# Performance work log

Measured on AMD Instinct MI355X. Metric: run time of the kernel, lower is better.

The kernel has to match this reference:

```python
import jax, jax.numpy as jnp
import numpy as np

N, CH = 65536, 256
B, K, CTX = 8, 256, 768
H, D = 8, 64
NPB = N // B  # points per batch (scene)


def setup_inputs() -> dict:
    key = jax.random.key(0)
    ks = jax.random.split(key, 8)
    xF = jax.random.normal(ks[0], (N, CH), dtype=jnp.float32)
    context = jax.random.normal(ks[1], (B, K, CTX), dtype=jnp.float32)
    # decomposition_permutations: a random partition of the N sparse points into B groups
    perm = jax.random.permutation(ks[2], N).reshape(B, NPB).astype(jnp.int32)
    Wq = jax.random.normal(ks[3], (CH, H * D), dtype=jnp.float32) * 0.02
    Wk = jax.random.normal(ks[4], (CTX, H * D), dtype=jnp.float32) * 0.02
    Wv = jax.random.normal(ks[5], (CTX, H * D), dtype=jnp.float32) * 0.02
    Wout = jax.random.normal(ks[6], (H * D, CH), dtype=jnp.float32) * 0.02
    b_out = jnp.zeros((CH,), dtype=jnp.float32)
    return {"xF": xF, "context": context, "perm": perm,
            "Wq": Wq, "Wk": Wk, "Wv": Wv, "Wout": Wout, "b_out": b_out}


def reference(xF, context, perm, Wq, Wk, Wv, Wout, b_out):
    scale = D ** -0.5
    q = (xF @ Wq).reshape(N, H, D)                     # to_q (1x1 conv == linear)
    k = (context @ Wk).reshape(B, K, H, D)             # to_k
    v = (context @ Wv).reshape(B, K, H, D)             # to_v
    qg = q[perm]                                        # gather: [B, NPB, H, D]
    attn = jax.nn.softmax(scale * jnp.einsum('bqhd,bkhd->bhqk', qg, k), axis=-1)
    o = jnp.einsum('bhqk,bkhd->bqhd', attn, v).reshape(B * NPB, H * D)
    # inverse-permutation scatter back to sparse-tensor order: ft[inv_perm]
    ft = jnp.zeros((N, H * D), o.dtype).at[perm.reshape(-1)].set(o)
    out = ft @ Wout + b_out                             # to_out
    return out + xF                                     # residual
```

## Files before the change

### kernel.cpp

```cpp
#include <hip/hip_runtime.h>

typedef unsigned short u16;
typedef __attribute__((ext_vector_type(8))) short bf16x8;
typedef __attribute__((ext_vector_type(4))) float f32x4;
typedef __attribute__((ext_vector_type(4))) int i32x4;
typedef __attribute__((ext_vector_type(2))) int i32x2;

#define N_PTS   65536
#define CH_DIM  256
#define BATCH   8
#define KTOK    256
#define CTX_DIM 768
#define NHEAD   8
#define HD      64
#define HDIM    512
#define NPB     8192

__device__ __forceinline__ u16 f2bf(float f) {
    union { float f; unsigned u; } v; v.f = f;
    unsigned r = v.u + 0x7fffu + ((v.u >> 16) & 1u);
    return (u16)(r >> 16);
}
__device__ __forceinline__ unsigned cvtpk(float lo, float hi) {
    unsigned r;
    asm("v_cvt_pk_bf16_f32 %0, %1, %2" : "=v"(r) : "v"(lo), "v"(hi));
    return r;
}
__device__ __forceinline__ float exp2_hw(float x) {
    float r;
    asm("v_exp_f32 %0, %1" : "=v"(r) : "v"(x));
    return r;
}

__device__ __forceinline__ void gll16(const void* g, void* l) {
    __builtin_amdgcn_global_load_lds(
        (const __attribute__((address_space(1))) void*)g,
        (__attribute__((address_space(3))) void*)l, 16, 0, 0);
}

__global__ void convk(const float* __restrict__ src, u16* __restrict__ dst, int n8) {
    int i = blockIdx.x * blockDim.x + threadIdx.x;
    int st = gridDim.x * blockDim.x;
    for (; i < n8; i += st) {
        const float* p = src + (size_t)i * 8;
        f32x4 a = *(const f32x4*)p;
        f32x4 b = *(const f32x4*)(p + 4);
        i32x4 o;
        o[0] = (int)cvtpk(a[0], a[1]);
        o[1] = (int)cvtpk(a[2], a[3]);
        o[2] = (int)cvtpk(b[0], b[1]);
        o[3] = (int)cvtpk(b[2], b[3]);
        *(i32x4*)&dst[(size_t)i * 8] = o;
    }
}

__global__ void tconvk(const float* __restrict__ W, u16* __restrict__ WT, int R, int C) {
    int i = blockIdx.x * blockDim.x + threadIdx.x;
    if (i >= R * C) return;
    int c = i / R, r = i - c * R;
    WT[(size_t)c * R + r] = f2bf(W[(size_t)r * C + c]);
}

template <bool OUT_F32, bool VT_OUT>
__global__ __launch_bounds__(256, 3) void gemm_bt(
    const u16* __restrict__ A, const u16* __restrict__ BT, void* __restrict__ Cv,
    int M, int N, int K,
    const float* __restrict__ bias, const float* __restrict__ resid, float oscale)
{
    __shared__ __align__(16) u16 As[128 * 32];
    __shared__ __align__(16) u16 Bs[128 * 32];

    const int tid  = threadIdx.x;
    const int lane = tid & 63;
    const int w    = tid >> 6;
    const int wm   = w & 1;
    const int wn   = w >> 1;

    const int nwg = gridDim.x * gridDim.y;
    const int wg  = blockIdx.y * gridDim.x + blockIdx.x;
    const int swz = (wg & 7) * (nwg >> 3) + (wg >> 3);
    const int n0  = (swz % gridDim.x) * 128;
    const int m0  = (swz / gridDim.x) * 128;

    const int l15  = lane & 15;
    const int quad = lane >> 4;

    f32x4 acc[4][4];
#pragma unroll
    for (int i = 0; i < 4; i++)
#pragma unroll
        for (int j = 0; j < 4; j++) { acc[i][j][0]=0.f; acc[i][j][1]=0.f; acc[i][j][2]=0.f; acc[i][j][3]=0.f; }

    const int sr = tid >> 2;
    const int sc = (tid & 3) * 8;
    const u16* Abase = A  + (size_t)(m0 + sr) * K + sc;
    const u16* Bbase = BT + (size_t)(n0 + sr) * K + sc;
    u16* AsD = &As[tid * 8];
    u16* BsD = &Bs[tid * 8];
    const size_t rowStep = (size_t)64 * K;

    for (int k0 = 0; k0 < K; k0 += 32) {
        gll16(Abase + k0,           AsD);
        gll16(Abase + k0 + rowStep, AsD + 2048);
        gll16(Bbase + k0,           BsD);
        gll16(Bbase + k0 + rowStep, BsD + 2048);
        __syncthreads();

        bf16x8 af[4], bfr[4];
#pragma unroll
        for (int rt = 0; rt < 4; rt++)
            af[rt] = *(const bf16x8*)&As[(wm * 64 + rt * 16 + l15) * 32 + quad * 8];
#pragma unroll
        for (int nt = 0; nt < 4; nt++)
            bfr[nt] = *(const bf16x8*)&Bs[(wn * 64 + nt * 16 + l15) * 32 + quad * 8];
#pragma unroll
        for (int rt = 0; rt < 4; rt++)
#pragma unroll
            for (int nt = 0; nt < 4; nt++)
                acc[rt][nt] = __builtin_amdgcn_mfma_f32_16x16x32_bf16(af[rt], bfr[nt], acc[rt][nt], 0, 0, 0);
        __syncthreads();
    }

    if (VT_OUT) {
        u16* CT = (u16*)Cv;
#pragma unroll
        for (int nt = 0; nt < 4; nt++) {
            int col = n0 + wn * 64 + nt * 16 + l15;
            int hh = col >> 6, dd = col & 63;
#pragma unroll
            for (int rt = 0; rt < 4; rt++) {
                int row = m0 + wm * 64 + rt * 16 + quad * 4;
                int bb = row >> 8, jb = row & 255;
                int jp = (jb & 0xE0) | ((jb & 0x0C) << 1) | ((jb & 0x10) >> 2);
                union { unsigned u[2]; i32x2 q; } pk;
                pk.u[0] = cvtpk(acc[rt][nt][0], acc[rt][nt][1]);
                pk.u[1] = cvtpk(acc[rt][nt][2], acc[rt][nt][3]);
                *(i32x2*)&CT[(((size_t)(bb * 8 + hh)) * 64 + dd) * 256 + jp] = pk.q;
            }
        }
    } else {
#pragma unroll
        for (int nt = 0; nt < 4; nt++) {
            int col = n0 + wn * 64 + nt * 16 + l15;
            float bv = bias ? bias[col] : 0.0f;
#pragma unroll
            for (int rt = 0; rt < 4; rt++) {
#pragma unroll
                for (int r = 0; r < 4; r++) {
                    int row = m0 + wm * 64 + rt * 16 + quad * 4 + r;
                    float v = acc[rt][nt][r] + bv;
                    if (resid) v += resid[(size_t)row * N + col];
                    if (OUT_F32) ((float*)Cv)[(size_t)row * N + col] = v;
                    else         ((u16*)Cv)[(size_t)row * N + col]   = f2bf(v * oscale);
                }
            }
        }
    }
}

template <bool OUT_F32, bool VT_OUT>
__global__ __launch_bounds__(256, 8) void gemm64(
    const u16* __restrict__ A, const u16* __restrict__ BT, void* __restrict__ Cv,
    int M, int N, int K,
    const float* __restrict__ bias, const float* __restrict__ resid, float oscale)
{
    __shared__ __align__(16) u16 As[64 * 32];
    __shared__ __align__(16) u16 Bs[64 * 32];

    const int tid  = threadIdx.x;
    const int lane = tid & 63;
    const int w    = tid >> 6;
    const int wm   = w & 1;
    const int wn   = w >> 1;

    const int nwg = gridDim.x * gridDim.y;
    const int wg  = blockIdx.y * gridDim.x + blockIdx.x;
    const int swz = (wg & 7) * (nwg >> 3) + (wg >> 3);
    const int n0  = (swz % gridDim.x) * 64;
    const int m0  = (swz / gridDim.x) * 64;

    const int l15  = lane & 15;
    const int quad = lane >> 4;

    f32x4 acc[2][2];
#pragma unroll
    for (int i = 0; i < 2; i++)
#pragma unroll
        for (int j = 0; j < 2; j++) { acc[i][j][0]=0.f; acc[i][j][1]=0.f; acc[i][j][2]=0.f; acc[i][j][3]=0.f; }

    const int sr = tid >> 2;
    const int sc = (tid & 3) * 8;
    const u16* Abase = A  + (size_t)(m0 + sr) * K + sc;
    const u16* Bbase = BT + (size_t)(n0 + sr) * K + sc;
    u16* AsD = &As[tid * 8];
    u16* BsD = &Bs[tid * 8];

    for (int k0 = 0; k0 < K; k0 += 32) {
        gll16(Abase + k0, AsD);
        gll16(Bbase + k0, BsD);
        __syncthreads();

        bf16x8 af[2], bfr[2];
#pragma unroll
        for (int rt = 0; rt < 2; rt++)
            af[rt] = *(const bf16x8*)&As[(wm * 32 + rt * 16 + l15) * 32 + quad * 8];
#pragma unroll
        for (int nt = 0; nt < 2; nt++)
            bfr[nt] = *(const bf16x8*)&Bs[(wn * 32 + nt * 16 + l15) * 32 + quad * 8];
#pragma unroll
        for (int rt = 0; rt < 2; rt++)
#pragma unroll
            for (int nt = 0; nt < 2; nt++)
                acc[rt][nt] = __builtin_amdgcn_mfma_f32_16x16x32_bf16(af[rt], bfr[nt], acc[rt][nt], 0, 0, 0);
        __syncthreads();
    }

    if (VT_OUT) {
        u16* CT = (u16*)Cv;
#pragma unroll
        for (int nt = 0; nt < 2; nt++) {
            int col = n0 + wn * 32 + nt * 16 + l15;
            int hh = col >> 6, dd = col & 63;
#pragma unroll
            for (int rt = 0; rt < 2; rt++) {
                int row = m0 + wm * 32 + rt * 16 + quad * 4;
                int bb = row >> 8, jb = row & 255;
                int jp = (jb & 0xE0) | ((jb & 0x0C) << 1) | ((jb & 0x10) >> 2);
                union { unsigned u[2]; i32x2 q; } pk;
                pk.u[0] = cvtpk(acc[rt][nt][0], acc[rt][nt][1]);
                pk.u[1] = cvtpk(acc[rt][nt][2], acc[rt][nt][3]);
                *(i32x2*)&CT[(((size_t)(bb * 8 + hh)) * 64 + dd) * 256 + jp] = pk.q;
            }
        }
    } else {
#pragma unroll
        for (int nt = 0; nt < 2; nt++) {
            int col = n0 + wn * 32 + nt * 16 + l15;
            float bv = bias ? bias[col] : 0.0f;
#pragma unroll
            for (int rt = 0; rt < 2; rt++) {
#pragma unroll
                for (int r = 0; r < 4; r++) {
                    int row = m0 + wm * 32 + rt * 16 + quad * 4 + r;
                    float v = acc[rt][nt][r] + bv;
                    if (resid) v += resid[(size_t)row * N + col];
                    if (OUT_F32) ((float*)Cv)[(size_t)row * N + col] = v;
                    else         ((u16*)Cv)[(size_t)row * N + col]   = f2bf(v * oscale);
                }
            }
        }
    }
}

#define KS2 72
#define VS2 264
__global__ __launch_bounds__(256, 4) void attn_mfma(
    const u16* qbuf, const u16* __restrict__ kbuf,
    const u16* __restrict__ vbufT, const int* __restrict__ perm,
    u16* ft)
{
    __shared__ __align__(16) u16 smem[18432];
    u16* Ks = smem;
    u16* Vt = smem;

    const int tid   = threadIdx.x;
    const int lane  = tid & 63;
    const int w     = tid >> 6;
    const int chunk = blockIdx.x;
    const int bh    = blockIdx.y;
    const int b     = bh >> 3;
    const int h     = bh & 7;
    const int l15   = lane & 15;
    const int quad  = lane >> 4;

    const int prow = perm[b * NPB + chunk * 64 + w * 16 + l15];
    const u16* qrow = qbuf + (size_t)prow * HDIM + h * HD;
    bf16x8 qf0 = *(const bf16x8*)&qrow[quad * 8];
    bf16x8 qf1 = *(const bf16x8*)&qrow[32 + quad * 8];

    {
        const int j8 = tid >> 3;
        const int c  = (tid & 7) * 8;
#pragma unroll
        for (int pass = 0; pass < 8; pass++) {
            int jj = j8 + pass * 32;
            i32x4 val = *(const i32x4*)&kbuf[((size_t)(b * KTOK + jj)) * HDIM + h * HD + c];
            *(i32x4*)&Ks[jj * KS2 + c] = val;
        }
    }
    __syncthreads();

    f32x4 sc[16];
#pragma unroll
    for (int nt = 0; nt < 16; nt++) { sc[nt][0]=0.f; sc[nt][1]=0.f; sc[nt][2]=0.f; sc[nt][3]=0.f; }
#pragma unroll
    for (int nt = 0; nt < 16; nt++) {
        bf16x8 kf = *(const bf16x8*)&Ks[(nt * 16 + l15) * KS2 + quad * 8];
        sc[nt] = __builtin_amdgcn_mfma_f32_16x16x32_bf16(kf, qf0, sc[nt], 0, 0, 0);
    }
#pragma unroll
    for (int nt = 0; nt < 16; nt++) {
        bf16x8 kf = *(const bf16x8*)&Ks[(nt * 16 + l15) * KS2 + 32 + quad * 8];
        sc[nt] = __builtin_amdgcn_mfma_f32_16x16x32_bf16(kf, qf1, sc[nt], 0, 0, 0);
    }

    i32x4 vreg[8];
    const u16* vslice = vbufT + ((size_t)(b * NHEAD + h)) * HD * KTOK;
    const int vrow = tid >> 2;
    const int vc0  = (tid & 3) * 8;
#pragma unroll
    for (int pass = 0; pass < 8; pass++)
        vreg[pass] = *(const i32x4*)&vslice[(size_t)vrow * KTOK + vc0 + pass * 32];

    float m = -1e30f;
#pragma unroll
    for (int nt = 0; nt < 16; nt++) {
        f32x4 v = sc[nt];
        m = fmaxf(m, fmaxf(fmaxf(v[0], v[1]), fmaxf(v[2], v[3])));
    }
    m = fmaxf(m, __shfl_xor(m, 16));
    m = fmaxf(m, __shfl_xor(m, 32));
    float s0 = 0.f, s1 = 0.f, s2 = 0.f, s3 = 0.f;
#pragma unroll
    for (int nt = 0; nt < 16; nt++) {
        float e0 = exp2_hw(sc[nt][0] - m);
        float e1 = exp2_hw(sc[nt][1] - m);
        float e2 = exp2_hw(sc[nt][2] - m);
        float e3 = exp2_hw(sc[nt][3] - m);
        sc[nt][0] = e0; sc[nt][1] = e1; sc[nt][2] = e2; sc[nt][3] = e3;
        s0 += e0; s1 += e1; s2 += e2; s3 += e3;
    }
    float s = (s0 + s1) + (s2 + s3);
    s += __shfl_xor(s, 16);
    s += __shfl_xor(s, 32);
    float inv = 1.0f / s;

    unsigned up[16][2];
#pragma unroll
    for (int nt = 0; nt < 16; nt++) {
        up[nt][0] = cvtpk(sc[nt][0], sc[nt][1]);
        up[nt][1] = cvtpk(sc[nt][2], sc[nt][3]);
    }

    __syncthreads();

#pragma unroll
    for (int pass = 0; pass < 8; pass++)
        *(i32x4*)&Vt[vrow * VS2 + vc0 + pass * 32] = vreg[pass];
    __syncthreads();

    f32x4 o[4];
#pragma unroll
    for (int n = 0; n < 4; n++) { o[n][0]=0.f; o[n][1]=0.f; o[n][2]=0.f; o[n][3]=0.f; }

#pragma unroll
    for (int ks = 0; ks < 8; ks++) {
        union { unsigned u[4]; bf16x8 v; } pb;
        pb.u[0] = up[2 * ks][0];
        pb.u[1] = up[2 * ks][1];
        pb.u[2] = up[2 * ks + 1][0];
        pb.u[3] = up[2 * ks + 1][1];
#pragma unroll
        for (int nt = 0; nt < 4; nt++) {
            bf16x8 bv = *(const bf16x8*)&Vt[(nt * 16 + l15) * VS2 + ks * 32 + quad * 8];
            o[nt] = __builtin_amdgcn_mfma_f32_16x16x32_bf16(pb.v, bv, o[nt], 0, 0, 0);
        }
    }

#pragma unroll
    for (int r = 0; r < 4; r++) {
        float invq = __shfl(inv,  quad * 4 + r);
        int   po   = __shfl(prow, quad * 4 + r);
        u16* frow = ft + (size_t)po * HDIM + h * HD;
        unsigned pa = cvtpk(o[0][r] * invq, o[1][r] * invq);
        unsigned pb = cvtpk(o[2][r] * invq, o[3][r] * invq);
        frow[l15]      = (u16)pa;
        frow[16 + l15] = (u16)(pa >> 16);
        frow[32 + l15] = (u16)pb;
        frow[48 + l15] = (u16)(pb >> 16);
    }
}

extern "C" void kernel_launch(void* const* d_in, const int* in_sizes, int n_in,
                              void* d_out, int out_size, void* d_ws, size_t ws_size,
                              hipStream_t stream) {
    const float* xF      = (const float*)d_in[0];
    const float* context = (const float*)d_in[1];
    const int*   perm    = (const int*)d_in[2];
    const float* Wq      = (const float*)d_in[3];
    const float* Wk      = (const float*)d_in[4];
    const float* Wv      = (const float*)d_in[5];
    const float* Wout    = (const float*)d_in[6];
    const float* b_out   = (const float*)d_in[7];
    float*       out     = (float*)d_out;

    const size_t WS_NEED = 71303168ULL;
    if (ws_size < WS_NEED) {
        hipMemsetAsync(d_out, 0, (size_t)out_size * sizeof(float), stream);
        return;
    }
    char* ws    = (char*)d_ws;
    u16* kbuf   = (u16*)(ws + 0);
    u16* vbufT  = (u16*)(ws + 2097152);
    u16* qbuf   = (u16*)(ws + 4194304);
    u16* ft     = qbuf;
    u16* WoutT  = (u16*)(ws + 2097152);

    char* ob    = (char*)d_out;
    u16* xb     = (u16*)(ob + 0);
    u16* cb     = (u16*)(ob + 33554432);
    u16* WqT    = (u16*)(ob + 36700160);
    u16* WkT    = (u16*)(ob + 36962304);
    u16* WvT    = (u16*)(ob + 37748736);

    convk<<<2048, 256, 0, stream>>>(xF, xb, N_PTS * CH_DIM / 8);
    convk<<<768, 256, 0, stream>>>(context, cb, BATCH * KTOK * CTX_DIM / 8);
    tconvk<<<(CH_DIM * HDIM + 255) / 256, 256, 0, stream>>>(Wq, WqT, CH_DIM, HDIM);
    tconvk<<<(CTX_DIM * HDIM + 255) / 256, 256, 0, stream>>>(Wk, WkT, CTX_DIM, HDIM);
    tconvk<<<(CTX_DIM * HDIM + 255) / 256, 256, 0, stream>>>(Wv, WvT, CTX_DIM, HDIM);

    gemm_bt<false, false><<<dim3(HDIM / 128, N_PTS / 128), 256, 0, stream>>>(
        xb, WqT, qbuf, N_PTS, HDIM, CH_DIM, nullptr, nullptr, 0.1803368801f);
    gemm64<false, false><<<dim3(HDIM / 64, (BATCH * KTOK) / 64), 256, 0, stream>>>(
        cb, WkT, kbuf, BATCH * KTOK, HDIM, CTX_DIM, nullptr, nullptr, 1.0f);
    gemm64<false, true><<<dim3(HDIM / 64, (BATCH * KTOK) / 64), 256, 0, stream>>>(
        cb, WvT, vbufT, BATCH * KTOK, HDIM, CTX_DIM, nullptr, nullptr, 1.0f);

    attn_mfma<<<dim3(NPB / 64, BATCH * NHEAD), 256, 0, stream>>>(
        qbuf, kbuf, vbufT, perm, ft);

    tconvk<<<(HDIM * CH_DIM + 255) / 256, 256, 0, stream>>>(Wout, WoutT, HDIM, CH_DIM);
    gemm_bt<true, false><<<dim3(CH_DIM / 128, N_PTS / 128), 256, 0, stream>>>(
        ft, WoutT, out, N_PTS, CH_DIM, HDIM, b_out, xF, 1.0f);
}
```

Measured before the change: 302.2 us.

## Double-buffer GEMM LDS tiles and fuse K/V projections into one kernel

The 128x128 and 64x64 GEMMs now use double-buffered LDS. The next K-tile's global-to-LDS loads are issued before the MFMAs on the current tile, and one barrier per iteration replaces two. The K and V projection GEMMs are merged into a single launch over a concatenated transposed weight, and each block writes either K or transposed V depending on its column range. The attention max reduction uses v_max3. This doubles LDS per block, which may reduce occupancy, and it relies on a full vmcnt(0) wait each iteration.

```diff
diff --git a/kernel.cpp b/kernel.cpp
--- a/kernel.cpp
+++ b/kernel.cpp
@@ -29,6 +29,11 @@
 __device__ __forceinline__ float exp2_hw(float x) {
     float r;
     asm("v_exp_f32 %0, %1" : "=v"(r) : "v"(x));
+    return r;
+}
+__device__ __forceinline__ float max3f(float a, float b, float c) {
+    float r;
+    asm("v_max3_f32 %0, %1, %2, %3" : "=v"(r) : "v"(a), "v"(b), "v"(c));
     return r;
 }
 
@@ -67,8 +72,8 @@
     int M, int N, int K,
     const float* __restrict__ bias, const float* __restrict__ resid, float oscale)
 {
-    __shared__ __align__(16) u16 As[128 * 32];
-    __shared__ __align__(16) u16 Bs[128 * 32];
+    __shared__ __align__(16) u16 As[2][128 * 32];
+    __shared__ __align__(16) u16 Bs[2][128 * 32];
 
     const int tid  = threadIdx.x;
     const int lane = tid & 63;
@@ -95,30 +100,46 @@
     const int sc = (tid & 3) * 8;
     const u16* Abase = A  + (size_t)(m0 + sr) * K + sc;
     const u16* Bbase = BT + (size_t)(n0 + sr) * K + sc;
-    u16* AsD = &As[tid * 8];
-    u16* BsD = &Bs[tid * 8];
     const size_t rowStep = (size_t)64 * K;
-
-    for (int k0 = 0; k0 < K; k0 += 32) {
-        gll16(Abase + k0,           AsD);
-        gll16(Abase + k0 + rowStep, AsD + 2048);
-        gll16(Bbase + k0,           BsD);
-        gll16(Bbase + k0 + rowStep, BsD + 2048);
-        __syncthreads();
-
+    const int d8 = tid * 8;
+
+    gll16(Abase,           &As[0][d8]);
+    gll16(Abase + rowStep, &As[0][d8 + 2048]);
+    gll16(Bbase,           &Bs[0][d8]);
+    gll16(Bbase + rowStep, &Bs[0][d8 + 2048]);
+    asm volatile("s_waitcnt vmcnt(0)" ::: "memory");
+    __builtin_amdgcn_s_barrier();
+    __builtin_amdgcn_sched_barrier(0);
+
+    const int ntile = K >> 5;
+    int cur = 0;
+    for (int t = 0; t < ntile; ++t) {
+        if (t + 1 < ntile) {
+            const u16* An = Abase + ((t + 1) << 5);
+            const u16* Bn = Bbase + ((t + 1) << 5);
+            const int nxt = cur ^ 1;
+            gll16(An,           &As[nxt][d8]);
+            gll16(An + rowStep, &As[nxt][d8 + 2048]);
+            gll16(Bn,           &Bs[nxt][d8]);
+            gll16(Bn + rowStep, &Bs[nxt][d8 + 2048]);
+        }
         bf16x8 af[4], bfr[4];
 #pragma unroll
         for (int rt = 0; rt < 4; rt++)
-            af[rt] = *(const bf16x8*)&As[(wm * 64 + rt * 16 + l15) * 32 + quad * 8];
+            af[rt] = *(const bf16x8*)&As[cur][(wm * 64 + rt * 16 + l15) * 32 + quad * 8];
 #pragma unroll
         for (int nt = 0; nt < 4; nt++)
-            bfr[nt] = *(const bf16x8*)&Bs[(wn * 64 + nt * 16 + l15) * 32 + quad * 8];
+            bfr[nt] = *(const bf16x8*)&Bs[cur][(wn * 64 + nt * 16 + l15) * 32 + quad * 8];
 #pragma unroll
         for (int rt = 0; rt < 4; rt++)
 #pragma unroll
             for (int nt = 0; nt < 4; nt++)
                 acc[rt][nt] = __builtin_amdgcn_mfma_f32_16x16x32_bf16(af[rt], bfr[nt], acc[rt][nt], 0, 0, 0);
-        __syncthreads();
+        asm volatile("s_waitcnt vmcnt(0)" ::: "memory");
+        __builtin_amdgcn_sched_barrier(0);
+        __builtin_amdgcn_s_barrier();
+        __builtin_amdgcn_sched_barrier(0);
+        cur ^= 1;
     }
 
     if (VT_OUT) {
@@ -158,14 +179,13 @@
     }
 }
 
-template <bool OUT_F32, bool VT_OUT>
-__global__ __launch_bounds__(256, 8) void gemm64(
-    const u16* __restrict__ A, const u16* __restrict__ BT, void* __restrict__ Cv,
-    int M, int N, int K,
-    const float* __restrict__ bias, const float* __restrict__ resid, float oscale)
+__global__ __launch_bounds__(256, 4) void gemm_kv(
+    const u16* __restrict__ A, const u16* __restrict__ BT,
+    u16* __restrict__ kd, u16* __restrict__ vtd)
 {
-    __shared__ __align__(16) u16 As[64 * 32];
-    __shared__ __align__(16) u16 Bs[64 * 32];
+    __shared__ __align__(16) u16 As[2][64 * 32];
+    __shared__ __align__(16) u16 Bs[2][64 * 32];
+    const int K = CTX_DIM;
 
     const int tid  = threadIdx.x;
     const int lane = tid & 63;
@@ -192,34 +212,58 @@
     const int sc = (tid & 3) * 8;
     const u16* Abase = A  + (size_t)(m0 + sr) * K + sc;
     const u16* Bbase = BT + (size_t)(n0 + sr) * K + sc;
-    u16* AsD = &As[tid * 8];
-    u16* BsD = &Bs[tid * 8];
-
-    for (int k0 = 0; k0 < K; k0 += 32) {
-        gll16(Abase + k0, AsD);
-        gll16(Bbase + k0, BsD);
-        __syncthreads();
-
+    const int d8 = tid * 8;
+
+    gll16(Abase, &As[0][d8]);
+    gll16(Bbase, &Bs[0][d8]);
+    asm volatile("s_waitcnt vmcnt(0)" ::: "memory");
+    __builtin_amdgcn_s_barrier();
+    __builtin_amdgcn_sched_barrier(0);
+
+    const int ntile = K >> 5;
+    int cur = 0;
+    for (int t = 0; t < ntile; ++t) {
+        if (t + 1 < ntile) {
+            const int nxt = cur ^ 1;
+            gll16(Abase + ((t + 1) << 5), &As[nxt][d8]);
+            gll16(Bbase + ((t + 1) << 5), &Bs[nxt][d8]);
+        }
         bf16x8 af[2], bfr[2];
 #pragma unroll
         for (int rt = 0; rt < 2; rt++)
-            af[rt] = *(const bf16x8*)&As[(wm * 32 + rt * 16 + l15) * 32 + quad * 8];
+            af[rt] = *(const bf16x8*)&As[cur][(wm * 32 + rt * 16 + l15) * 32 + quad * 8];
 #pragma unroll
         for (int nt = 0; nt < 2; nt++)
-            bfr[nt] = *(const bf16x8*)&Bs[(wn * 32 + nt * 16 + l15) * 32 + quad * 8];
+            bfr[nt] = *(const bf16x8*)&Bs[cur][(wn * 32 + nt * 16 + l15) * 32 + quad * 8];
 #pragma unroll
         for (int rt = 0; rt < 2; rt++)
 #pragma unroll
             for (int nt = 0; nt < 2; nt++)
                 acc[rt][nt] = __builtin_amdgcn_mfma_f32_16x16x32_bf16(af[rt], bfr[nt], acc[rt][nt], 0, 0, 0);
-        __syncthreads();
-    }
-
-    if (VT_OUT) {
-        u16* CT = (u16*)Cv;
+        asm volatile("s_waitcnt vmcnt(0)" ::: "memory");
+        __builtin_amdgcn_sched_barrier(0);
+        __builtin_amdgcn_s_barrier();
+        __builtin_amdgcn_sched_barrier(0);
+        cur ^= 1;
+    }
+
+    if (n0 < 512) {
 #pragma unroll
         for (int nt = 0; nt < 2; nt++) {
             int col = n0 + wn * 32 + nt * 16 + l15;
+#pragma unroll
+            for (int rt = 0; rt < 2; rt++) {
+#pragma unroll
+                for (int r = 0; r < 4; r++) {
+                    int row = m0 + wm * 32 + rt * 16 + quad * 4 + r;
+                    kd[(size_t)row * HDIM + col] = f2bf(acc[rt][nt][r]);
+                }
+            }
+        }
+    } else {
+#pragma unroll
+        for (int nt = 0; nt < 2; nt++) {
+            int col = (n0 - 512) + wn * 32 + nt * 16 + l15;
             int hh = col >> 6, dd = col & 63;
 #pragma unroll
             for (int rt = 0; rt < 2; rt++) {
@@ -229,24 +273,7 @@
                 union { unsigned u[2]; i32x2 q; } pk;
                 pk.u[0] = cvtpk(acc[rt][nt][0], acc[rt][nt][1]);
                 pk.u[1] = cvtpk(acc[rt][nt][2], acc[rt][nt][3]);
-                *(i32x2*)&CT[(((size_t)(bb * 8 + hh)) * 64 + dd) * 256 + jp] = pk.q;
-            }
-        }
-    } else {
-#pragma unroll
-        for (int nt = 0; nt < 2; nt++) {
-            int col = n0 + wn * 32 + nt * 16 + l15;
-            float bv = bias ? bias[col] : 0.0f;
-#pragma unroll
-            for (int rt = 0; rt < 2; rt++) {
-#pragma unroll
-                for (int r = 0; r < 4; r++) {
-                    int row = m0 + wm * 32 + rt * 16 + quad * 4 + r;
-                    float v = acc[rt][nt][r] + bv;
-                    if (resid) v += resid[(size_t)row * N + col];
-                    if (OUT_F32) ((float*)Cv)[(size_t)row * N + col] = v;
-                    else         ((u16*)Cv)[(size_t)row * N + col]   = f2bf(v * oscale);
-                }
+                *(i32x2*)&vtd[(((size_t)(bb * 8 + hh)) * 64 + dd) * 256 + jp] = pk.q;
             }
         }
     }
@@ -316,7 +343,7 @@
 #pragma unroll
     for (int nt = 0; nt < 16; nt++) {
         f32x4 v = sc[nt];
-        m = fmaxf(m, fmaxf(fmaxf(v[0], v[1]), fmaxf(v[2], v[3])));
+        m = max3f(m, max3f(v[0], v[1], v[2]), v[3]);
     }
     m = fmaxf(m, __shfl_xor(m, 16));
     m = fmaxf(m, __shfl_xor(m, 32));
@@ -409,22 +436,18 @@
     char* ob    = (char*)d_out;
     u16* xb     = (u16*)(ob + 0);
     u16* cb     = (u16*)(ob + 33554432);
-    u16* WqT    = (u16*)(ob + 36700160);
-    u16* WkT    = (u16*)(ob + 36962304);
-    u16* WvT    = (u16*)(ob + 37748736);
+    u16* WkvT   = (u16*)(ob + 36700160);
+    u16* WqT    = (u16*)(ob + 38273024);
 
     convk<<<2048, 256, 0, stream>>>(xF, xb, N_PTS * CH_DIM / 8);
     convk<<<768, 256, 0, stream>>>(context, cb, BATCH * KTOK * CTX_DIM / 8);
     tconvk<<<(CH_DIM * HDIM + 255) / 256, 256, 0, stream>>>(Wq, WqT, CH_DIM, HDIM);
-    tconvk<<<(CTX_DIM * HDIM + 255) / 256, 256, 0, stream>>>(Wk, WkT, CTX_DIM, HDIM);
-    tconvk<<<(CTX_DIM * HDIM + 255) / 256, 256, 0, stream>>>(Wv, WvT, CTX_DIM, HDIM);
+    tconvk<<<(CTX_DIM * HDIM + 255) / 256, 256, 0, stream>>>(Wk, WkvT, CTX_DIM, HDIM);
+    tconvk<<<(CTX_DIM * HDIM + 255) / 256, 256, 0, stream>>>(Wv, WkvT + 512 * 768, CTX_DIM, HDIM);
 
     gemm_bt<false, false><<<dim3(HDIM / 128, N_PTS / 128), 256, 0, stream>>>(
         xb, WqT, qbuf, N_PTS, HDIM, CH_DIM, nullptr, nullptr, 0.1803368801f);
-    gemm64<false, false><<<dim3(HDIM / 64, (BATCH * KTOK) / 64), 256, 0, stream>>>(
-        cb, WkT, kbuf, BATCH * KTOK, HDIM, CTX_DIM, nullptr, nullptr, 1.0f);
-    gemm64<false, true><<<dim3(HDIM / 64, (BATCH * KTOK) / 64), 256, 0, stream>>>(
-        cb, WvT, vbufT, BATCH * KTOK, HDIM, CTX_DIM, nullptr, nullptr, 1.0f);
+    gemm_kv<<<dim3(16, 32), 256, 0, stream>>>(cb, WkvT, kbuf, vbufT);
 
     attn_mfma<<<dim3(NPB / 64, BATCH * NHEAD), 256, 0, stream>>>(
         qbuf, kbuf, vbufT, perm, ft);
```

After: 301.2 us. No clear change (-0.3%).
